# Optimization experiments

Hardware: AMD Instinct MI355X
Metric: run time of the kernel (lower is better)

## Reference

```python
import jax, jax.numpy as jnp
import numpy as np
from jax import lax

N_NODES = 100000
N_EDGES = 3200000
K = 10
ALPHA = 0.1


def setup_inputs() -> dict:
    key = jax.random.key(0)
    ks = jax.random.split(key, 6)
    x = jax.random.normal(ks[0], (N_NODES, 500), dtype=jnp.float32)
    edge_index = jax.random.randint(ks[1], (2, N_EDGES), 0, N_NODES, dtype=jnp.int64)
    W1 = jax.random.normal(ks[2], (500, 256), dtype=jnp.float32) * (1.0 / np.sqrt(500))
    b1 = jax.random.normal(ks[3], (256,), dtype=jnp.float32) * 0.01
    W2 = jax.random.normal(ks[4], (256, 64), dtype=jnp.float32) * (1.0 / np.sqrt(256))
    b2 = jax.random.normal(ks[5], (64,), dtype=jnp.float32) * 0.01
    return {"x": x, "edge_index": edge_index, "W1": W1, "b1": b1, "W2": W2, "b2": b2}


def reference(x, edge_index, W1, b1, W2, b2):
    N = x.shape[0]
    # MLP encoder (eval mode: dropout is identity)
    h = jnp.maximum(x @ W1 + b1, 0.0)
    h = h @ W2 + b2  # [N, out_channels]

    # APPNP with GCN normalization + self-loops (PyG default)
    loops = jnp.arange(N, dtype=edge_index.dtype)
    row = jnp.concatenate([edge_index[0], loops])  # source nodes
    col = jnp.concatenate([edge_index[1], loops])  # target nodes
    deg = jax.ops.segment_sum(jnp.ones(row.shape[0], dtype=h.dtype), col, num_segments=N)
    dinv = jnp.where(deg > 0, deg ** -0.5, 0.0)
    norm = dinv[row] * dinv[col]  # [E+N]

    def step(z, _):
        agg = jax.ops.segment_sum(norm[:, None] * z[row], col, num_segments=N)
        z = (1.0 - ALPHA) * agg + ALPHA * h
        return z, None

    z, _ = lax.scan(step, h, None, length=K)
    return jax.nn.log_softmax(z, axis=1)
```

## Files before the change

### kernel.cpp

```cpp
#include <hip/hip_runtime.h>
#include <hip/hip_bf16.h>

#define N_NODES 100000
#define N_EDGES 3200000
#define KITER   10
#define ALPHA   0.1f

#define SCAN_BS 512
#define SCAN_NB ((N_NODES + SCAN_BS - 1) / SCAN_BS)

#define NSUB    256
#define SEGCAP  2048
#define OVCAP   262144
#define CB_EDGES 1024
#define CB_CAP   256
#define NWIN    128
#define WN      98
#define SB_CAP  48
#define SUBCAP  4096

typedef __attribute__((ext_vector_type(4))) float f32x4;
typedef __attribute__((ext_vector_type(8))) short bf16x8;
typedef __attribute__((ext_vector_type(4))) unsigned int u32x4;
typedef unsigned short u16;
typedef unsigned int u32;

__device__ inline float bf2f(u16 u) {
    unsigned int x = ((unsigned int)u) << 16;
    return __uint_as_float(x);
}
__device__ inline float bf2f_lo(unsigned int w) { return __uint_as_float(w << 16); }
__device__ inline float bf2f_hi(unsigned int w) { return __uint_as_float(w & 0xffff0000u); }
__device__ inline u16 f2bf(float f) {
    __hip_bfloat16 h = __float2bfloat16(f);
    return *reinterpret_cast<u16*>(&h);
}
__device__ inline bf16x8 cvt8(float4 lo, float4 hi) {
    bf16x8 r;
    r[0] = (short)f2bf(lo.x); r[1] = (short)f2bf(lo.y);
    r[2] = (short)f2bf(lo.z); r[3] = (short)f2bf(lo.w);
    r[4] = (short)f2bf(hi.x); r[5] = (short)f2bf(hi.y);
    r[6] = (short)f2bf(hi.z); r[7] = (short)f2bf(hi.w);
    return r;
}
__device__ inline void glds16(const u16* g, u16* l) {
    __builtin_amdgcn_global_load_lds(
        (const __attribute__((address_space(1))) u32*)g,
        (__attribute__((address_space(3))) u32*)l, 16, 0, 0);
}

__global__ void k_detect(const unsigned int* e32, int* flag) {
    if (threadIdx.x == 0) {
        int is64 = 1;
        for (int i = 0; i < 64; ++i)
            if (e32[2 * i + 1] != 0u) { is64 = 0; break; }
        *flag = is64;
    }
}

__device__ inline int eidx(const void* p, int is64, int i) {
    if (is64) return (int)((const long long*)p)[i];
    return ((const int*)p)[i];
}

__global__ __launch_bounds__(256) void k_convert_bucket3(
    const void* edges, const int* flag,
    unsigned int* __restrict__ buckets, int* __restrict__ bcur,
    int2* __restrict__ ovf, int* __restrict__ ovfn) {
    __shared__ unsigned int lbuf[8][CB_CAP];
    __shared__ int lcnt[8];
    __shared__ int lbase[8];
    int t = threadIdx.x;
    if (t < 8) lcnt[t] = 0;
    __syncthreads();
    int e0 = blockIdx.x * CB_EDGES;
    int is64 = *flag;
#pragma unroll
    for (int j = 0; j < CB_EDGES / 256; ++j) {
        int i = e0 + j * 256 + t;
        int r = eidx(edges, is64, i);
        int c = eidx(edges, is64, N_EDGES + i);
        int b = c / 12500;
        int coff = c - b * 12500;
        unsigned int pack = ((unsigned)coff << 17) | (unsigned)r;
        int pos = atomicAdd(&lcnt[b], 1);
        if (pos < CB_CAP) {
            lbuf[b][pos] = pack;
        } else {
            int op = atomicAdd(ovfn, 1);
            if (op < OVCAP) ovf[op] = make_int2(c, r);
        }
    }
    __syncthreads();
    int sub = blockIdx.x & (NSUB - 1);
    if (t < 8) {
        int n = min(lcnt[t], CB_CAP);
        lbase[t] = atomicAdd(&bcur[t * NSUB + sub], n);
    }
    __syncthreads();
#pragma unroll
    for (int bb = 0; bb < 8; ++bb) {
        int n = min(lcnt[bb], CB_CAP);
        int base = lbase[bb];
        size_t segoff = ((size_t)(bb * NSUB + sub)) * SEGCAP;
        for (int i = t; i < n; i += 256) {
            int pos = base + i;
            unsigned int pk = lbuf[bb][i];
            if (pos < SEGCAP) {
                buckets[segoff + pos] = pk;
            } else {
                int c = bb * 12500 + (int)(pk >> 17);
                int r = (int)(pk & 0x1FFFFu);
                int op = atomicAdd(ovfn, 1);
                if (op < OVCAP) ovf[op] = make_int2(c, r);
            }
        }
    }
}

__global__ __launch_bounds__(256) void k_subpart(
    const unsigned int* __restrict__ buckets, const int* __restrict__ bcur,
    unsigned int* __restrict__ subbuck, int* __restrict__ scur,
    int2* __restrict__ ovf, int* __restrict__ ovfn) {
    __shared__ unsigned int sbin[NWIN][SB_CAP];
    __shared__ int scnt[NWIN];
    __shared__ int sbase[NWIN];
    int t = threadIdx.x;
    int b = blockIdx.x & 7;
    int sub = blockIdx.x >> 3;
    int idx = b * NSUB + sub;
    if (t < NWIN) scnt[t] = 0;
    __syncthreads();
    int n = min(bcur[idx], SEGCAP);
    const unsigned int* bk = buckets + (size_t)idx * SEGCAP;
    for (int e = t; e < n; e += 256) {
        unsigned int pk = bk[e];
        int j = (int)(pk >> 17) / WN;
        int p = atomicAdd(&scnt[j], 1);
        if (p < SB_CAP) {
            sbin[j][p] = pk;
        } else {
            int c = b * 12500 + (int)(pk >> 17);
            int r = (int)(pk & 0x1FFFFu);
            int op = atomicAdd(ovfn, 1);
            if (op < OVCAP) ovf[op] = make_int2(c, r);
        }
    }
    __syncthreads();
    if (t < NWIN) {
        int cnt = min(scnt[t], SB_CAP);
        sbase[t] = atomicAdd(&scur[b * NWIN + t], cnt);
    }
    __syncthreads();
    for (int i = t; i < NWIN * SB_CAP; i += 256) {
        int j = i / SB_CAP, s = i % SB_CAP;
        if (s < min(scnt[j], SB_CAP)) {
            int pos = sbase[j] + s;
            unsigned int pk = sbin[j][s];
            if (pos < SUBCAP) {
                subbuck[((size_t)(b * NWIN + j)) * SUBCAP + pos] = pk;
            } else {
                int c = b * 12500 + (int)(pk >> 17);
                int r = (int)(pk & 0x1FFFFu);
                int op = atomicAdd(ovfn, 1);
                if (op < OVCAP) ovf[op] = make_int2(c, r);
            }
        }
    }
}

__global__ __launch_bounds__(256) void k_deghist2(const unsigned int* __restrict__ subbuck,
                                                  const int* __restrict__ scur,
                                                  int* __restrict__ deg) {
    __shared__ int h[WN];
    int t = threadIdx.x;
    int b = blockIdx.x & 7;
    int j = blockIdx.x >> 3;
    int base_node = b * 12500 + j * WN;
    int nn = min(WN, 12500 - j * WN);
    if (t < WN) h[t] = 0;
    __syncthreads();
    int idx = b * NWIN + j;
    int n = min(scur[idx], SUBCAP);
    const unsigned int* sb = subbuck + (size_t)idx * SUBCAP;
    for (int e = t; e < n; e += 256)
        atomicAdd(&h[(int)(sb[e] >> 17) - j * WN], 1);
    __syncthreads();
    if (t < nn) deg[base_node + t] = h[t];
}

__global__ void k_deg_ovf(const int2* __restrict__ ovf, const int* __restrict__ ovfn,
                          int* deg) {
    int n = min(*ovfn, OVCAP);
    for (int i = blockIdx.x * 256 + threadIdx.x; i < n; i += gridDim.x * 256)
        atomicAdd(&deg[ovf[i].x], 1);
}

__global__ __launch_bounds__(SCAN_BS) void k_scan_part(const int* __restrict__ deg,
                                                       int* __restrict__ ptr,
                                                       int* __restrict__ bsum) {
    __shared__ int lds[SCAN_BS];
    int t = threadIdx.x;
    int idx = blockIdx.x * SCAN_BS + t;
    int s = (idx < N_NODES) ? deg[idx] : 0;
    lds[t] = s;
    __syncthreads();
#pragma unroll
    for (int off = 1; off < SCAN_BS; off <<= 1) {
        int v = (t >= off) ? lds[t - off] : 0;
        __syncthreads();
        lds[t] += v;
        __syncthreads();
    }
    if (idx < N_NODES) ptr[idx] = lds[t] - s;
    if (t == SCAN_BS - 1) bsum[blockIdx.x] = lds[t];
}

__global__ __launch_bounds__(256) void k_scan_bsum(const int* __restrict__ bsum,
                                                   int* __restrict__ boff,
                                                   int* __restrict__ ptr) {
    __shared__ int lds[256];
    int t = threadIdx.x;
    int s = (t < SCAN_NB) ? bsum[t] : 0;
    lds[t] = s;
    __syncthreads();
#pragma unroll
    for (int off = 1; off < 256; off <<= 1) {
        int v = (t >= off) ? lds[t - off] : 0;
        __syncthreads();
        lds[t] += v;
        __syncthreads();
    }
    if (t < SCAN_NB) boff[t] = lds[t] - s;
    if (t == 255) ptr[N_NODES] = lds[t];
}

__global__ __launch_bounds__(SCAN_BS) void k_scan_apply(const int* __restrict__ deg,
                                                        const int* __restrict__ boff,
                                                        int* __restrict__ ptr,
                                                        int* __restrict__ cursor,
                                                        float* __restrict__ dinv) {
    int idx = blockIdx.x * SCAN_BS + threadIdx.x;
    if (idx >= N_NODES) return;
    int p = ptr[idx] + boff[blockIdx.x];
    ptr[idx] = p;
    cursor[idx] = p;
    dinv[idx] = rsqrtf((float)(deg[idx] + 1));
}

__global__ __launch_bounds__(256) void k_fill6(const unsigned int* __restrict__ subbuck,
                                               const int* __restrict__ scur,
                                               const int* __restrict__ ptr,
                                               int* __restrict__ cursor,
                                               int* __restrict__ csr_src) {
    __shared__ int lcur[WN];
    int t = threadIdx.x;
    int b = blockIdx.x & 7;
    int j = blockIdx.x >> 3;
    int base_node = b * 12500 + j * WN;
    int nn = min(WN, 12500 - j * WN);
    if (t < nn) lcur[t] = ptr[base_node + t];
    __syncthreads();
    int idx = b * NWIN + j;
    int n = min(scur[idx], SUBCAP);
    const unsigned int* sb = subbuck + (size_t)idx * SUBCAP;
    for (int e = t; e < n; e += 256) {
        unsigned int pk = sb[e];
        int local = (int)(pk >> 17) - j * WN;
        int r = (int)(pk & 0x1FFFFu);
        int pos = atomicAdd(&lcur[local], 1);
        csr_src[pos] = r;
    }
    __syncthreads();
    if (t < nn) cursor[base_node + t] = lcur[t];
}

__global__ void k_fill_ovf(const int2* __restrict__ ovf, const int* __restrict__ ovfn,
                           int* cursor, int* __restrict__ csr_src) {
    int n = min(*ovfn, OVCAP);
    for (int i = blockIdx.x * 256 + threadIdx.x; i < n; i += gridDim.x * 256) {
        int2 e = ovf[i];
        csr_src[atomicAdd(&cursor[e.x], 1)] = e.y;
    }
}

__global__ void k_wconv1(const float* W1, u16* W1s) {
    int idx = blockIdx.x * 256 + threadIdx.x;
    if (idx >= 16 * 256 * 32) return;
    int ks = idx / (256 * 32);
    int rem = idx % (256 * 32);
    int n = rem / 32, kk = rem % 32;
    int k = ks * 32 + kk;
    float v = (k < 500) ? W1[k * 256 + n] : 0.0f;
    int slot = kk >> 3, kl = kk & 7;
    int sslot = slot ^ ((n >> 1) & 3);
    W1s[ks * 8192 + n * 32 + sslot * 8 + kl] = f2bf(v);
}

__global__ void k_wconv2(const float* W2, u16* W2s) {
    int idx = blockIdx.x * 256 + threadIdx.x;
    if (idx >= 8 * 64 * 32) return;
    int ks = idx / (64 * 32);
    int rem = idx % (64 * 32);
    int n = rem / 32, kk = rem % 32;
    int k = ks * 32 + kk;
    W2s[idx] = f2bf(W2[k * 64 + n]);
}

#define MLP2_ROWS 128
#define HSTR 264
#define H2STR 72

__global__ __launch_bounds__(512, 4) void k_mlp2(
    const float* __restrict__ x, const u16* __restrict__ W1s,
    const float* __restrict__ b1, const u16* __restrict__ W2s,
    const float* __restrict__ b2, const float* __restrict__ dinv,
    u16* __restrict__ h_bf, u16* __restrict__ zs0) {

    __shared__ u16 smem[33792];
    u16* Abuf = smem;
    u16* Bbuf = smem + 8192;

    int t = threadIdx.x;
    int lane = t & 63, w = t >> 6;
    int wr = w >> 2, wc = w & 3;
    int cl = lane & 15, hi = lane >> 4;
    int m0 = blockIdx.x * MLP2_ROWS;

    int sr = t >> 2, skq = t & 3;
    int srow = min(m0 + sr, N_NODES - 1);
    const size_t XMAX = (size_t)N_NODES * 500 - 4;
    size_t sbase = (size_t)srow * 500 + skq * 8;
    int sAoff = sr * 32 + ((skq ^ ((sr >> 1) & 3)) << 3);

    f32x4 acc[4][4];
    f32x4 zero = {0.f, 0.f, 0.f, 0.f};
#pragma unroll
    for (int nt = 0; nt < 4; ++nt)
#pragma unroll
        for (int i = 0; i < 4; ++i) acc[nt][i] = zero;

    float4 pa, pb;

    {
        size_t f = sbase;
        size_t a0 = f > XMAX ? XMAX : f;
        size_t a1 = (f + 4) > XMAX ? XMAX : (f + 4);
        pa = *(const float4*)(x + a0);
        pb = *(const float4*)(x + a1);
        glds16(W1s + (w * 2 + 0) * 512 + lane * 8, Bbuf + (w * 2 + 0) * 512);
        glds16(W1s + (w * 2 + 1) * 512 + lane * 8, Bbuf + (w * 2 + 1) * 512);
        bf16x8 av = cvt8(pa, pb);
        *(bf16x8*)&Abuf[sAoff] = av;
    }
    __syncthreads();

    for (int ks = 0; ks < 16; ++ks) {
        int cur = ks & 1, nxt = cur ^ 1;
        if (ks < 15) {
            size_t f = sbase + (size_t)(ks + 1) * 32;
            size_t a0 = f > XMAX ? XMAX : f;
            size_t a1 = (f + 4) > XMAX ? XMAX : (f + 4);
            pa = *(const float4*)(x + a0);
            pb = *(const float4*)(x + a1);
            const u16* bsrc = W1s + (ks + 1) * 8192;
            glds16(bsrc + (w * 2 + 0) * 512 + lane * 8,
                   Bbuf + nxt * 8192 + (w * 2 + 0) * 512);
            glds16(bsrc + (w * 2 + 1) * 512 + lane * 8,
                   Bbuf + nxt * 8192 + (w * 2 + 1) * 512);
        }
        const u16* Ab = Abuf + cur * 4096;
        const u16* Bb = Bbuf + cur * 8192;
        bf16x8 af[4];
#pragma unroll
        for (int i = 0; i < 4; ++i) {
            int row = wr * 64 + i * 16 + cl;
            af[i] = *(const bf16x8*)&Ab[row * 32 + ((hi ^ ((row >> 1) & 3)) << 3)];
        }
#pragma unroll
        for (int nt = 0; nt < 4; ++nt) {
            int n = wc * 64 + nt * 16 + cl;
            bf16x8 bv = *(const bf16x8*)&Bb[n * 32 + ((hi ^ ((n >> 1) & 3)) << 3)];
#pragma unroll
            for (int i = 0; i < 4; ++i)
                acc[nt][i] = __builtin_amdgcn_mfma_f32_16x16x32_bf16(af[i], bv, acc[nt][i], 0, 0, 0);
        }
        if (ks < 15) {
            bf16x8 av = cvt8(pa, pb);
            *(bf16x8*)&Abuf[nxt * 4096 + sAoff] = av;
        }
        __syncthreads();
    }

    u16* H = smem;
#pragma unroll
    for (int nt = 0; nt < 4; ++nt) {
        int col = wc * 64 + nt * 16 + cl;
        float bb = b1[col];
#pragma unroll
        for (int i = 0; i < 4; ++i) {
            int row = wr * 64 + i * 16 + hi * 4;
#pragma unroll
            for (int r = 0; r < 4; ++r)
                H[(row + r) * HSTR + col] = f2bf(fmaxf(acc[nt][i][r] + bb, 0.0f));
        }
    }
    __syncthreads();

    f32x4 acc2[4];
#pragma unroll
    for (int i = 0; i < 4; ++i) acc2[i] = zero;
    int rA0 = w * 16 + cl;
#pragma unroll
    for (int ks2 = 0; ks2 < 8; ++ks2) {
        bf16x8 afv = *(const bf16x8*)&H[rA0 * HSTR + ks2 * 32 + 8 * hi];
#pragma unroll
        for (int nt = 0; nt < 4; ++nt) {
            bf16x8 bv = *(const bf16x8*)(W2s + (ks2 * 64 + nt * 16 + cl) * 32 + 8 * hi);
            acc2[nt] = __builtin_amdgcn_mfma_f32_16x16x32_bf16(afv, bv, acc2[nt], 0, 0, 0);
        }
    }
    __syncthreads();

    u16* H2 = smem;
    {
        int rl0 = w * 16 + hi * 4;
#pragma unroll
        for (int nt = 0; nt < 4; ++nt) {
            int col = nt * 16 + cl;
            float bb = b2[col];
#pragma unroll
            for (int r = 0; r < 4; ++r)
                H2[(rl0 + r) * H2STR + col] = f2bf(acc2[nt][r] + bb);
        }
    }
    __syncthreads();

    {
        int rl = t >> 2, q = t & 3;
        int grow = m0 + rl;
        if (grow < N_NODES) {
            float dv = dinv[grow];
            const u32x4* src = (const u32x4*)&H2[rl * H2STR + q * 16];
            u32x4 hq[2] = {src[0], src[1]};
            u32x4 zq[2];
#pragma unroll
            for (int i = 0; i < 2; ++i) {
#pragma unroll
                for (int jj = 0; jj < 4; ++jj) {
                    unsigned int hw = hq[i][jj];
                    float lo = dv * bf2f_lo(hw);
                    float hi2 = dv * bf2f_hi(hw);
                    zq[i][jj] = (unsigned)f2bf(lo) | ((unsigned)f2bf(hi2) << 16);
                }
            }
            u32x4* hd = (u32x4*)(h_bf + (size_t)grow * 64 + q * 16);
            u32x4* zd = (u32x4*)(zs0 + (size_t)grow * 64 + q * 16);
            hd[0] = hq[0]; hd[1] = hq[1];
            zd[0] = zq[0]; zd[1] = zq[1];
        }
    }
}

__global__ __launch_bounds__(256) void k_prop3(
    const u16* __restrict__ zs_in, const u16* __restrict__ h_bf,
    const float* __restrict__ dinv, const int* __restrict__ ptr,
    const int* __restrict__ csr_src, u16* __restrict__ zs_out,
    float* __restrict__ out, int last) {

    int lane = threadIdx.x & 63;
    int g = lane >> 3;
    int c = lane & 7;
    int v = blockIdx.x * 4 + (threadIdx.x >> 6);
    if (v >= N_NODES) return;
    int s0 = ptr[v], s1 = ptr[v + 1];

    float a0 = 0.f, a1 = 0.f, a2 = 0.f, a3 = 0.f;
    float a4 = 0.f, a5 = 0.f, a6 = 0.f, a7 = 0.f;
    float b0 = 0.f, b1 = 0.f, b2 = 0.f, b3 = 0.f;
    float b4 = 0.f, b5 = 0.f, b6 = 0.f, b7 = 0.f;

    for (int base = s0; base < s1; base += 64) {
        int nwin = min(64, s1 - base);
        int ei = base + lane;
        int sv = (ei < s1) ? csr_src[ei] : v;
        int j = 0;
        for (; j + 16 <= nwin; j += 16) {
            int u0 = __shfl(sv, j + g, 64);
            int u1 = __shfl(sv, j + 8 + g, 64);
            u32x4 q0 = *(const u32x4*)(zs_in + (size_t)u0 * 64 + c * 8);
            u32x4 q1 = *(const u32x4*)(zs_in + (size_t)u1 * 64 + c * 8);
            a0 += bf2f_lo(q0.x); a1 += bf2f_hi(q0.x);
            a2 += bf2f_lo(q0.y); a3 += bf2f_hi(q0.y);
            a4 += bf2f_lo(q0.z); a5 += bf2f_hi(q0.z);
            a6 += bf2f_lo(q0.w); a7 += bf2f_hi(q0.w);
            b0 += bf2f_lo(q1.x); b1 += bf2f_hi(q1.x);
            b2 += bf2f_lo(q1.y); b3 += bf2f_hi(q1.y);
            b4 += bf2f_lo(q1.z); b5 += bf2f_hi(q1.z);
            b6 += bf2f_lo(q1.w); b7 += bf2f_hi(q1.w);
        }
        for (; j < nwin; j += 8) {
            int idx = j + g;
            int u = __shfl(sv, idx, 64);
            u32x4 q = *(const u32x4*)(zs_in + (size_t)u * 64 + c * 8);
            if (idx < nwin) {
                a0 += bf2f_lo(q.x); a1 += bf2f_hi(q.x);
                a2 += bf2f_lo(q.y); a3 += bf2f_hi(q.y);
                a4 += bf2f_lo(q.z); a5 += bf2f_hi(q.z);
                a6 += bf2f_lo(q.w); a7 += bf2f_hi(q.w);
            }
        }
    }
    a0 += b0; a1 += b1; a2 += b2; a3 += b3;
    a4 += b4; a5 += b5; a6 += b6; a7 += b7;
#pragma unroll
    for (int off = 8; off <= 32; off <<= 1) {
        a0 += __shfl_xor(a0, off, 64); a1 += __shfl_xor(a1, off, 64);
        a2 += __shfl_xor(a2, off, 64); a3 += __shfl_xor(a3, off, 64);
        a4 += __shfl_xor(a4, off, 64); a5 += __shfl_xor(a5, off, 64);
        a6 += __shfl_xor(a6, off, 64); a7 += __shfl_xor(a7, off, 64);
    }

    float dv = dinv[v];
    u32x4 qs = *(const u32x4*)(zs_in + (size_t)v * 64 + c * 8);
    u32x4 qh = *(const u32x4*)(h_bf + (size_t)v * 64 + c * 8);
    float z0 = (1.0f - ALPHA) * dv * (a0 + bf2f_lo(qs.x)) + ALPHA * bf2f_lo(qh.x);
    float z1 = (1.0f - ALPHA) * dv * (a1 + bf2f_hi(qs.x)) + ALPHA * bf2f_hi(qh.x);
    float z2 = (1.0f - ALPHA) * dv * (a2 + bf2f_lo(qs.y)) + ALPHA * bf2f_lo(qh.y);
    float z3 = (1.0f - ALPHA) * dv * (a3 + bf2f_hi(qs.y)) + ALPHA * bf2f_hi(qh.y);
    float z4 = (1.0f - ALPHA) * dv * (a4 + bf2f_lo(qs.z)) + ALPHA * bf2f_lo(qh.z);
    float z5 = (1.0f - ALPHA) * dv * (a5 + bf2f_hi(qs.z)) + ALPHA * bf2f_hi(qh.z);
    float z6 = (1.0f - ALPHA) * dv * (a6 + bf2f_lo(qs.w)) + ALPHA * bf2f_lo(qh.w);
    float z7 = (1.0f - ALPHA) * dv * (a7 + bf2f_hi(qs.w)) + ALPHA * bf2f_hi(qh.w);

    if (!last) {
        if (g == 0) {
            u32x4 o;
            o.x = (unsigned)f2bf(dv * z0) | ((unsigned)f2bf(dv * z1) << 16);
            o.y = (unsigned)f2bf(dv * z2) | ((unsigned)f2bf(dv * z3) << 16);
            o.z = (unsigned)f2bf(dv * z4) | ((unsigned)f2bf(dv * z5) << 16);
            o.w = (unsigned)f2bf(dv * z6) | ((unsigned)f2bf(dv * z7) << 16);
            *(u32x4*)(zs_out + (size_t)v * 64 + c * 8) = o;
        }
    } else {
        float m = fmaxf(fmaxf(fmaxf(z0, z1), fmaxf(z2, z3)),
                        fmaxf(fmaxf(z4, z5), fmaxf(z6, z7)));
#pragma unroll
        for (int off = 1; off <= 4; off <<= 1) m = fmaxf(m, __shfl_xor(m, off, 64));
        float p = expf(z0 - m) + expf(z1 - m) + expf(z2 - m) + expf(z3 - m)
                + expf(z4 - m) + expf(z5 - m) + expf(z6 - m) + expf(z7 - m);
#pragma unroll
        for (int off = 1; off <= 4; off <<= 1) p += __shfl_xor(p, off, 64);
        float ls = logf(p);
        if (g == 0) {
            f32x4 o1 = {z0 - m - ls, z1 - m - ls, z2 - m - ls, z3 - m - ls};
            f32x4 o2 = {z4 - m - ls, z5 - m - ls, z6 - m - ls, z7 - m - ls};
            *(f32x4*)(out + (size_t)v * 64 + c * 8) = o1;
            *(f32x4*)(out + (size_t)v * 64 + c * 8 + 4) = o2;
        }
    }
}

extern "C" void kernel_launch(void* const* d_in, const int* in_sizes, int n_in,
                              void* d_out, int out_size, void* d_ws, size_t ws_size,
                              hipStream_t stream) {
    const float* x  = (const float*)d_in[0];
    const void* edges = d_in[1];
    const float* W1 = (const float*)d_in[2];
    const float* b1 = (const float*)d_in[3];
    const float* W2 = (const float*)d_in[4];
    const float* b2 = (const float*)d_in[5];
    float* out = (float*)d_out;

    char* ws = (char*)d_ws;
    size_t off = 0;
    auto alloc = [&](size_t bytes) -> void* {
        void* p = ws + off;
        off = (off + bytes + 255) & ~(size_t)255;
        return p;
    };
    int*   flag    = (int*)alloc(4);
    int*   deg     = (int*)alloc((size_t)N_NODES * 4);
    float* dinv    = (float*)alloc((size_t)N_NODES * 4);
    int*   ptr     = (int*)alloc((size_t)(N_NODES + 1) * 4);
    int*   cursor  = (int*)alloc((size_t)N_NODES * 4);
    int*   bsum    = (int*)alloc((size_t)SCAN_NB * 4);
    int*   boff    = (int*)alloc((size_t)SCAN_NB * 4);
    int*   csr_src = (int*)alloc((size_t)N_EDGES * 4);
    u16*   W1s     = (u16*)alloc((size_t)16 * 256 * 32 * 2);
    u16*   W2s     = (u16*)alloc((size_t)8 * 64 * 32 * 2);
    u16*   h_bf    = (u16*)alloc((size_t)N_NODES * 64 * 2);
    u16*   zsA     = (u16*)alloc((size_t)N_NODES * 64 * 2);
    u32*   buckets = (u32*)alloc((size_t)8 * NSUB * SEGCAP * 4);
    u32*   subbuck = (u32*)alloc((size_t)8 * NWIN * SUBCAP * 4);
    int*   bctl    = (int*)alloc((size_t)(8 * NSUB + 8 * NWIN + 16) * 4);
    int2*  ovf     = (int2*)alloc((size_t)OVCAP * 8);
    u16*   zsB     = (u16*)subbuck;

    int* bcur = bctl;
    int* scur = bctl + 8 * NSUB;
    int* ovfn = bctl + 8 * NSUB + 8 * NWIN;

    hipMemsetAsync(deg, 0, (size_t)N_NODES * 4, stream);
    hipMemsetAsync(bctl, 0, (size_t)(8 * NSUB + 8 * NWIN + 16) * 4, stream);
    k_detect<<<1, 64, 0, stream>>>((const unsigned int*)edges, flag);
    k_convert_bucket3<<<N_EDGES / CB_EDGES, 256, 0, stream>>>(edges, flag,
                                                              buckets, bcur, ovf, ovfn);
    k_subpart<<<8 * NSUB, 256, 0, stream>>>(buckets, bcur, subbuck, scur, ovf, ovfn);
    k_deghist2<<<8 * NWIN, 256, 0, stream>>>(subbuck, scur, deg);
    k_deg_ovf<<<32, 256, 0, stream>>>(ovf, ovfn, deg);
    k_scan_part<<<SCAN_NB, SCAN_BS, 0, stream>>>(deg, ptr, bsum);
    k_scan_bsum<<<1, 256, 0, stream>>>(bsum, boff, ptr);
    k_scan_apply<<<SCAN_NB, SCAN_BS, 0, stream>>>(deg, boff, ptr, cursor, dinv);
    k_fill6<<<8 * NWIN, 256, 0, stream>>>(subbuck, scur, ptr, cursor, csr_src);
    k_fill_ovf<<<64, 256, 0, stream>>>(ovf, ovfn, cursor, csr_src);
    k_wconv1<<<(16 * 256 * 32 + 255) / 256, 256, 0, stream>>>(W1, W1s);
    k_wconv2<<<(8 * 64 * 32 + 255) / 256, 256, 0, stream>>>(W2, W2s);
    k_mlp2<<<(N_NODES + MLP2_ROWS - 1) / MLP2_ROWS, 512, 0, stream>>>(x, W1s, b1, W2s, b2,
                                                                      dinv, h_bf, zsA);

    const u16* zin = zsA;
    u16* zout = zsB;
    for (int k = 0; k < KITER; ++k) {
        int last = (k == KITER - 1) ? 1 : 0;
        k_prop3<<<(N_NODES + 3) / 4, 256, 0, stream>>>(zin, h_bf, dinv, ptr, csr_src,
                                                       zout, out, last);
        u16* t = zout;
        zout = (u16*)zin;
        zin = t;
    }
}
```

Measured before the change: 710.7 us.

## Triple-buffer MLP GEMM k-loop with explicit vmcnt waits for deeper prefetch

Deepens the first-layer MLP GEMM pipeline from double to triple buffering. The x tile and W1 slice are prefetched two k-steps ahead. Full __syncthreads is replaced by hand-placed s_waitcnt vmcnt counts, sched barriers and raw s_barrier, which aims to hide global-load latency behind the MFMAs. Shared memory grows, and the hard-coded wait counts depend on the exact number of issued loads, so occupancy or correctness could suffer if the compiler reorders memory ops.

```diff
diff --git a/kernel.cpp b/kernel.cpp
--- a/kernel.cpp
+++ b/kernel.cpp
@@ -24,6 +24,10 @@
 typedef __attribute__((ext_vector_type(4))) unsigned int u32x4;
 typedef unsigned short u16;
 typedef unsigned int u32;
+
+#define WAITV(N) asm volatile("s_waitcnt vmcnt(" #N ")" ::: "memory")
+#define WAITL0   asm volatile("s_waitcnt lgkmcnt(0)" ::: "memory")
+#define MEMFENCE asm volatile("" ::: "memory")
 
 __device__ inline float bf2f(u16 u) {
     unsigned int x = ((unsigned int)u) << 16;
@@ -317,9 +321,9 @@
     const float* __restrict__ b2, const float* __restrict__ dinv,
     u16* __restrict__ h_bf, u16* __restrict__ zs0) {
 
-    __shared__ u16 smem[33792];
+    __shared__ u16 smem[36864];
     u16* Abuf = smem;
-    u16* Bbuf = smem + 8192;
+    u16* Bbuf = smem + 12288;
 
     int t = threadIdx.x;
     int lane = t & 63, w = t >> 6;
@@ -340,37 +344,58 @@
 #pragma unroll
         for (int i = 0; i < 4; ++i) acc[nt][i] = zero;
 
-    float4 pa, pb;
+    float4 xs[2][2];
 
     {
-        size_t f = sbase;
-        size_t a0 = f > XMAX ? XMAX : f;
-        size_t a1 = (f + 4) > XMAX ? XMAX : (f + 4);
-        pa = *(const float4*)(x + a0);
-        pb = *(const float4*)(x + a1);
+        size_t f0 = sbase;
+        size_t a0 = f0 > XMAX ? XMAX : f0;
+        size_t a1 = (f0 + 4) > XMAX ? XMAX : (f0 + 4);
+        float4 p0 = *(const float4*)(x + a0);
+        float4 p1 = *(const float4*)(x + a1);
+        MEMFENCE;
         glds16(W1s + (w * 2 + 0) * 512 + lane * 8, Bbuf + (w * 2 + 0) * 512);
         glds16(W1s + (w * 2 + 1) * 512 + lane * 8, Bbuf + (w * 2 + 1) * 512);
-        bf16x8 av = cvt8(pa, pb);
+        MEMFENCE;
+        size_t f1 = sbase + 32;
+        size_t b0 = f1 > XMAX ? XMAX : f1;
+        size_t b1a = (f1 + 4) > XMAX ? XMAX : (f1 + 4);
+        xs[1][0] = *(const float4*)(x + b0);
+        xs[1][1] = *(const float4*)(x + b1a);
+        MEMFENCE;
+        const u16* bs1 = W1s + 8192;
+        glds16(bs1 + (w * 2 + 0) * 512 + lane * 8, Bbuf + 8192 + (w * 2 + 0) * 512);
+        glds16(bs1 + (w * 2 + 1) * 512 + lane * 8, Bbuf + 8192 + (w * 2 + 1) * 512);
+        WAITV(6);
+        __builtin_amdgcn_sched_barrier(0);
+        bf16x8 av = cvt8(p0, p1);
         *(bf16x8*)&Abuf[sAoff] = av;
-    }
-    __syncthreads();
-
+        WAITL0;
+        __builtin_amdgcn_s_barrier();
+    }
+
+#pragma unroll
     for (int ks = 0; ks < 16; ++ks) {
-        int cur = ks & 1, nxt = cur ^ 1;
-        if (ks < 15) {
-            size_t f = sbase + (size_t)(ks + 1) * 32;
+        const int b_cur = ks % 3, b_wr = (ks + 1) % 3, b_pf = (ks + 2) % 3;
+        if (ks + 2 <= 15) {
+            size_t f = sbase + (size_t)(ks + 2) * 32;
             size_t a0 = f > XMAX ? XMAX : f;
             size_t a1 = (f + 4) > XMAX ? XMAX : (f + 4);
-            pa = *(const float4*)(x + a0);
-            pb = *(const float4*)(x + a1);
-            const u16* bsrc = W1s + (ks + 1) * 8192;
+            xs[ks & 1][0] = *(const float4*)(x + a0);
+            xs[ks & 1][1] = *(const float4*)(x + a1);
+            MEMFENCE;
+            const u16* bsrc = W1s + (ks + 2) * 8192;
             glds16(bsrc + (w * 2 + 0) * 512 + lane * 8,
-                   Bbuf + nxt * 8192 + (w * 2 + 0) * 512);
+                   Bbuf + b_pf * 8192 + (w * 2 + 0) * 512);
             glds16(bsrc + (w * 2 + 1) * 512 + lane * 8,
-                   Bbuf + nxt * 8192 + (w * 2 + 1) * 512);
-        }
-        const u16* Ab = Abuf + cur * 4096;
-        const u16* Bb = Bbuf + cur * 8192;
+                   Bbuf + b_pf * 8192 + (w * 2 + 1) * 512);
+            MEMFENCE;
+        }
+        if (ks <= 13)      { WAITV(8); }
+        else if (ks == 14) { WAITV(4); }
+        else               { WAITV(0); }
+        __builtin_amdgcn_sched_barrier(0);
+        const u16* Ab = Abuf + b_cur * 4096;
+        const u16* Bb = Bbuf + b_cur * 8192;
         bf16x8 af[4];
 #pragma unroll
         for (int i = 0; i < 4; ++i) {
@@ -385,11 +410,14 @@
             for (int i = 0; i < 4; ++i)
                 acc[nt][i] = __builtin_amdgcn_mfma_f32_16x16x32_bf16(af[i], bv, acc[nt][i], 0, 0, 0);
         }
-        if (ks < 15) {
-            bf16x8 av = cvt8(pa, pb);
-            *(bf16x8*)&Abuf[nxt * 4096 + sAoff] = av;
-        }
-        __syncthreads();
+        if (ks <= 14) {
+            if (ks <= 13) { WAITV(6); } else { WAITV(2); }
+            __builtin_amdgcn_sched_barrier(0);
+            bf16x8 av = cvt8(xs[(ks + 1) & 1][0], xs[(ks + 1) & 1][1]);
+            *(bf16x8*)&Abuf[b_wr * 4096 + sAoff] = av;
+        }
+        WAITL0;
+        __builtin_amdgcn_s_barrier();
     }
 
     u16* H = smem;
```

New measurement: 726.8 us. 2.3% more time.
